# Kernel tuning notes

Hardware: AMD Instinct MI355X
Metric: run time of the kernel (lower is better)

## Reference

```python
import jax, jax.numpy as jnp
import numpy as np

# Model dims (see shape_source): seq_len fixed to 12 by reshape(1,12,-1); rnn_units fixed to 64 by proj in-dim.
B, T, N, HZ = 16, 12, 512, 12
DIN, DOUT, YCOV = 1, 1, 1
RNN, MEMN, MEMD, K = 64, 20, 64, 3
DDEC = RNN + MEMD  # 128


def _cheb(g, k):
    # Chebyshev polynomials T_0..T_{k-1} of support g: [I, g, 2g T_{i-1} - T_{i-2}, ...]
    n = g.shape[0]
    Ts = [jnp.eye(n, dtype=g.dtype), g]
    for _ in range(2, k):
        Ts.append(2.0 * g @ Ts[-1] - Ts[-2])
    return Ts


def _agcn(x, sup, W, b):
    # x: [B,N,C], sup: [2K,N,N] -> x_g: [B,N,2K*C] (k-major order matches torch.cat over support_set)
    b_, n, _ = x.shape
    xg = jnp.einsum('knm,bmc->bnkc', sup, x).reshape(b_, n, -1)
    return xg @ W + b


def _cell(x, state, sup, gW, gb, uW, ub, hdim):
    ins = jnp.concatenate([x, state], axis=-1)
    zr = jax.nn.sigmoid(_agcn(ins, sup, gW, gb))
    z, r = zr[..., :hdim], zr[..., hdim:]
    hc = jnp.tanh(_agcn(jnp.concatenate([x, z * state], axis=-1), sup, uW, ub))
    return r * state + (1.0 - r) * hc


def setup_inputs() -> dict:
    key = jax.random.key(0)
    ks = jax.random.split(key, 16)
    def nrm(k, shape, s=0.1):
        return jax.random.normal(k, shape, dtype=jnp.float32) * s
    return {
        'x': nrm(ks[0], (B, T, N, DIN), 1.0),
        'y_cov': nrm(ks[1], (B, HZ, N, YCOV), 1.0),
        'Memory': nrm(ks[2], (MEMN, MEMD)),
        'Wq': nrm(ks[3], (RNN, MEMD)),
        'We1': nrm(ks[4], (N, MEMN)),
        'We2': nrm(ks[5], (N, MEMN)),
        'tWe1': nrm(ks[6], (MEMD, RNN)),
        'tWe2': nrm(ks[7], (MEMD, RNN)),
        'fc_d_W': nrm(ks[8], (DDEC, RNN)),
        'fc_e_W': nrm(ks[9], (RNN, RNN)),
        'enc_gate_W': nrm(ks[10], (2 * K * (DIN + RNN), 2 * RNN)),
        'enc_gate_b': jnp.zeros((2 * RNN,), jnp.float32),
        'enc_up_W': nrm(ks[11], (2 * K * (DIN + RNN), RNN)),
        'enc_up_b': jnp.zeros((RNN,), jnp.float32),
        'dec_gate_W': nrm(ks[12], (2 * K * (DOUT + YCOV + DDEC), 2 * DDEC)),
        'dec_gate_b': jnp.zeros((2 * DDEC,), jnp.float32),
        'dec_up_W': nrm(ks[13], (2 * K * (DOUT + YCOV + DDEC), DDEC)),
        'dec_up_b': jnp.zeros((DDEC,), jnp.float32),
        'proj_W': nrm(ks[14], (DDEC + RNN, DOUT)),
        'proj_b': jnp.zeros((DOUT,), jnp.float32),
    }


def reference(x, y_cov, Memory, Wq, We1, We2, tWe1, tWe2, fc_d_W, fc_e_W,
              enc_gate_W, enc_gate_b, enc_up_W, enc_up_b,
              dec_gate_W, dec_gate_b, dec_up_W, dec_up_b, proj_W, proj_b):
    # adaptive supports from memory
    ne1 = We1 @ Memory
    ne2 = We2 @ Memory
    g1 = jax.nn.softmax(jax.nn.relu(ne1 @ ne2.T), axis=-1)
    g2 = jax.nn.softmax(jax.nn.relu(ne2 @ ne1.T), axis=-1)
    sup = jnp.stack(_cheb(g1, K) + _cheb(g2, K))  # [2K,N,N]

    # encoder: GRU-style graph recurrence over time via scan
    def enc_step(state, xt):
        h = _cell(xt, state, sup, enc_gate_W, enc_gate_b, enc_up_W, enc_up_b, RNN)
        return h, h
    s0 = jnp.zeros((B, N, RNN), x.dtype)
    _, hs = jax.lax.scan(enc_step, s0, jnp.swapaxes(x, 0, 1))
    h_en = jnp.swapaxes(hs, 0, 1)  # [B,T,N,RNN]
    h_t = h_en[:, -1]

    # memory retrieval
    query = h_t @ Wq                                    # [B,N,MEMD]
    att_score = jax.nn.softmax(query @ Memory.T, axis=-1)  # [B,N,MEMN]
    h_att = att_score @ Memory                          # [B,N,MEMD]
    _, ind = jax.lax.top_k(att_score, 20)
    pos = Memory[ind[:, :, 0]]
    neg = Memory[ind[:, :, 1:]]

    # test-time supports from last-batch retrieved memory (as in torch code: h_att[-1])
    ne3 = h_att[-1] @ tWe1
    ne4 = h_att[-1] @ tWe2
    tg1 = jax.nn.softmax(jax.nn.relu(ne3 @ ne4.T), axis=-1)
    tg2 = jax.nn.softmax(jax.nn.relu(ne4 @ ne3.T), axis=-1)
    tsup = jnp.stack(_cheb(tg1, K) + _cheb(tg2, K))

    ht = jnp.concatenate([h_t, h_att], axis=-1)  # [B,N,DDEC]
    # matches torch fc_e(h_en).reshape(1,12,-1): row-major flatten of [B,T,N,RNN] into [T, B*N*RNN]
    e_flat = (h_en @ fc_e_W).reshape(T, -1)

    go = jnp.zeros((B, N, DOUT), x.dtype)
    state = ht  # num_layers = 1
    outs = []
    for t in range(HZ):
        xt = jnp.concatenate([go, y_cov[:, t]], axis=-1)
        h_de = _cell(xt, state, tsup, dec_gate_W, dec_gate_b, dec_up_W, dec_up_b, DDEC)
        state = h_de
        d_flat = (h_de @ fc_d_W).reshape(-1)            # [B*N*RNN]
        att = jax.nn.softmax(e_flat @ d_flat)           # [T] global temporal weights
        context = jnp.einsum('btnr,t->bnr', h_en, att)  # [B,N,RNN]
        go = jnp.concatenate([h_de, context], axis=-1) @ proj_W + proj_b
        outs.append(go)
    output = jnp.stack(outs, axis=1)  # [B,HZ,N,DOUT]
    return output, h_att, query, pos, neg, att_score
```

## Files before the change

kernel.cpp:

```cpp
#include <hip/hip_runtime.h>
#include <hip/hip_bf16.h>
#include <math.h>

typedef __hip_bfloat16 bf16;
typedef __attribute__((ext_vector_type(8))) short short8;
typedef __attribute__((ext_vector_type(4))) float f32x4;
typedef unsigned short u16;

__device__ inline u16 f2bu(float f) {
  unsigned u = __builtin_bit_cast(unsigned, f);
  u += 0x7fffu + ((u >> 16) & 1u);
  return (u16)(u >> 16);
}

__global__ void detect_k(const u16* __restrict__ u, int* __restrict__ flag) {
  if (threadIdx.x == 0 && blockIdx.x == 0) {
    int wild = 0;
    for (int i = 0; i < 256; i++) {
      int e = (u[i] >> 7) & 0xFF;
      if (e < 0x66 || e > 0x8A) wild++;
    }
    *flag = (wild > 64) ? 1 : 0;
  }
}

__global__ void in2f_k(const void* __restrict__ in, float* __restrict__ out, int n,
                       const int* __restrict__ flag) {
  int i = blockIdx.x * 256 + threadIdx.x;
  if (i >= n) return;
  if (*flag) out[i] = ((const float*)in)[i];
  else       out[i] = __bfloat162float(((const bf16*)in)[i]);
}

__global__ void zero_k(float* __restrict__ p, int n) {
  int i = blockIdx.x * 256 + threadIdx.x;
  if (i < n) p[i] = 0.f;
}

__global__ void zeroi_k(int* __restrict__ p, int n) {
  int i = blockIdx.x * 256 + threadIdx.x;
  if (i < n) p[i] = 0;
}

__global__ void transpose_k(const float* __restrict__ in, float* __restrict__ out,
                            int rows, int cols) {
  int i = blockIdx.x * 256 + threadIdx.x;
  if (i >= rows * cols) return;
  int c = i % cols, r = i / cols;
  out[(size_t)c * rows + r] = in[i];
}

__global__ void f2b_k(const float* __restrict__ in, u16* __restrict__ out, int n) {
  int i = blockIdx.x * 256 + threadIdx.x;
  if (i < n) out[i] = f2bu(in[i]);
}

__global__ void padw_k(const float* __restrict__ W, float* __restrict__ Wp,
                       int K, int N, int Kpad) {
  int i = blockIdx.x * 256 + threadIdx.x;
  if (i >= Kpad * N) return;
  int n = i % N, k = i / N;
  Wp[i] = (k < K) ? W[(size_t)k * N + n] : 0.f;
}

__global__ void w2bt_k(const float* __restrict__ W, u16* __restrict__ WT,
                       int KT, int Nw, int KTpad) {
  int i = blockIdx.x * 256 + threadIdx.x;
  if (i >= Nw * KTpad) return;
  int kp = i % KTpad, n = i / KTpad;
  WT[i] = (kp < KT) ? f2bu(W[(size_t)kp * Nw + n]) : (u16)0;
}

enum { EPI_NONE = 0, EPI_RELU = 1, EPI_SIG = 2, EPI_CHEB = 3, EPI_SCAT = 4, EPI_UPD = 5 };

struct GemmArgs {
  const float* A; const float* Bm; float* C;
  int M, N, K;
};
__global__ __launch_bounds__(256) void gemm_s(GemmArgs g) {
  __shared__ float As[16][65];
  __shared__ float Bs[16][65];
  const int tid = threadIdx.x;
  const int tx = tid & 15, ty = tid >> 4;
  const int bm = blockIdx.y * 64, bn = blockIdx.x * 64;
  float acc[4][4] = {{0.f}};
  for (int k0 = 0; k0 < g.K; k0 += 16) {
#pragma unroll
    for (int i = 0; i < 4; i++) {
      int idx = i * 256 + tid; int c = idx & 15, r = idx >> 4;
      int mm = bm + r, kk = k0 + c;
      As[c][r] = (mm < g.M && kk < g.K) ? g.A[(size_t)mm * g.K + kk] : 0.f;
    }
#pragma unroll
    for (int i = 0; i < 4; i++) {
      int idx = i * 256 + tid; int c = idx & 63, r = idx >> 6;
      int kk = k0 + r, nn = bn + c;
      Bs[r][c] = (kk < g.K && nn < g.N) ? g.Bm[(size_t)kk * g.N + nn] : 0.f;
    }
    __syncthreads();
#pragma unroll
    for (int kk = 0; kk < 16; kk++) {
      float a[4], b[4];
#pragma unroll
      for (int i = 0; i < 4; i++) a[i] = As[kk][ty * 4 + i];
#pragma unroll
      for (int j = 0; j < 4; j++) b[j] = Bs[kk][tx * 4 + j];
#pragma unroll
      for (int i = 0; i < 4; i++)
#pragma unroll
        for (int j = 0; j < 4; j++) acc[i][j] = fmaf(a[i], b[j], acc[i][j]);
    }
    __syncthreads();
  }
#pragma unroll
  for (int i = 0; i < 4; i++) {
    int m = bm + ty * 4 + i;
    if (m >= g.M) continue;
#pragma unroll
    for (int j = 0; j < 4; j++) {
      int n = bn + tx * 4 + j;
      if (n >= g.N) continue;
      g.C[(size_t)m * g.N + n] = acc[i][j];
    }
  }
}

struct FGemmArgs {
  const float* A; const float* Bm; const float* bias; float* C;
  int M, N, K, ldb;
  const float* aux0;
  float* aux1;
  float* aux2;
  float* aux3;
  float* aux4;
  int i0, i1, i2;
};

template<int EPI>
__global__ __launch_bounds__(256) void fgemm_k(FGemmArgs g) {
  __shared__ __align__(16) float As[2][32][68];
  __shared__ __align__(16) float Bs[2][32][68];
  const int tid = threadIdx.x;
  const int tx = tid & 15, ty = tid >> 4;
  const int bm = blockIdx.y * 64, bn = blockIdx.x * 64;
  const int ar = tid >> 2, ac = (tid & 3) * 4;
  const int br = tid >> 4, bc = (tid & 15) * 4;
  float acc[4][4] = {{0.f}};

  float4 av0 = *(const float4*)(g.A + (size_t)(bm + ar) * g.K + ac);
  float4 av1 = *(const float4*)(g.A + (size_t)(bm + ar) * g.K + 16 + ac);
  float4 bv0 = *(const float4*)(g.Bm + (size_t)br * g.ldb + bn + bc);
  float4 bv1 = *(const float4*)(g.Bm + (size_t)(16 + br) * g.ldb + bn + bc);
  As[0][ac + 0][ar] = av0.x; As[0][ac + 1][ar] = av0.y;
  As[0][ac + 2][ar] = av0.z; As[0][ac + 3][ar] = av0.w;
  As[0][16 + ac + 0][ar] = av1.x; As[0][16 + ac + 1][ar] = av1.y;
  As[0][16 + ac + 2][ar] = av1.z; As[0][16 + ac + 3][ar] = av1.w;
  *(float4*)&Bs[0][br][bc] = bv0;
  *(float4*)&Bs[0][16 + br][bc] = bv1;
  __syncthreads();

  int cur = 0;
  for (int k0 = 0; k0 < g.K; k0 += 32) {
    const bool has_next = (k0 + 32 < g.K);
    if (has_next) {
      av0 = *(const float4*)(g.A + (size_t)(bm + ar) * g.K + k0 + 32 + ac);
      av1 = *(const float4*)(g.A + (size_t)(bm + ar) * g.K + k0 + 48 + ac);
      bv0 = *(const float4*)(g.Bm + (size_t)(k0 + 32 + br) * g.ldb + bn + bc);
      bv1 = *(const float4*)(g.Bm + (size_t)(k0 + 48 + br) * g.ldb + bn + bc);
    }
#pragma unroll
    for (int kk = 0; kk < 32; kk++) {
      float4 a4 = *(const float4*)&As[cur][kk][ty * 4];
      float4 b4 = *(const float4*)&Bs[cur][kk][tx * 4];
      float a[4] = {a4.x, a4.y, a4.z, a4.w};
      float b[4] = {b4.x, b4.y, b4.z, b4.w};
#pragma unroll
      for (int i = 0; i < 4; i++)
#pragma unroll
        for (int j = 0; j < 4; j++) acc[i][j] = fmaf(a[i], b[j], acc[i][j]);
    }
    if (has_next) {
      int nxt = cur ^ 1;
      As[nxt][ac + 0][ar] = av0.x; As[nxt][ac + 1][ar] = av0.y;
      As[nxt][ac + 2][ar] = av0.z; As[nxt][ac + 3][ar] = av0.w;
      As[nxt][16 + ac + 0][ar] = av1.x; As[nxt][16 + ac + 1][ar] = av1.y;
      As[nxt][16 + ac + 2][ar] = av1.z; As[nxt][16 + ac + 3][ar] = av1.w;
      *(float4*)&Bs[nxt][br][bc] = bv0;
      *(float4*)&Bs[nxt][16 + br][bc] = bv1;
      __syncthreads();
      cur = nxt;
    }
  }
#pragma unroll
  for (int i = 0; i < 4; i++) {
    int m = bm + ty * 4 + i;
#pragma unroll
    for (int j = 0; j < 4; j++) {
      int n = bn + tx * 4 + j;
      if (n >= g.N) continue;
      float v = acc[i][j];
      if (EPI == EPI_NONE) {
        g.C[(size_t)m * g.N + n] = v;
      } else if (EPI == EPI_RELU) {
        g.C[(size_t)m * g.N + n] = fmaxf(v, 0.f);
      } else if (EPI == EPI_CHEB) {
        g.C[(size_t)m * g.N + n] = 2.f * v - (m == n ? 1.f : 0.f);
      } else if (EPI == EPI_SCAT) {
        int bb = n / g.i0, cc = n % g.i0;
        int km = m >> 9;
        int kmap = km + 1 + (km >= 2 ? 1 : 0);
        int node = m & 511;
        g.aux1[((size_t)bb * 512 + node) * g.i1 + (size_t)kmap * g.i0 + cc] = v;
      }
    }
  }
}

template<int EPI>
__global__ __launch_bounds__(256) void fgemm32_k(FGemmArgs g) {
  __shared__ __align__(16) float As[2][16][40];
  __shared__ __align__(16) float Bs[2][16][68];
  const int tid = threadIdx.x;
  const int tx = tid & 15, ty = tid >> 4;
  const int bm = blockIdx.y * 32, bn = blockIdx.x * 64;
  const int ar = tid >> 2, ac = (tid & 3) * 4;
  const int br = tid >> 4, bc = (tid & 15) * 4;
  float acc[2][4] = {{0.f}};

  float4 av, bv;
  if (ar < 32) av = *(const float4*)(g.A + (size_t)(bm + ar) * g.K + ac);
  bv = *(const float4*)(g.Bm + (size_t)br * g.ldb + bn + bc);
  if (ar < 32) {
    As[0][ac + 0][ar] = av.x; As[0][ac + 1][ar] = av.y;
    As[0][ac + 2][ar] = av.z; As[0][ac + 3][ar] = av.w;
  }
  *(float4*)&Bs[0][br][bc] = bv;
  __syncthreads();

  int cur = 0;
  for (int k0 = 0; k0 < g.K; k0 += 16) {
    const bool has_next = (k0 + 16 < g.K);
    if (has_next) {
      if (ar < 32) av = *(const float4*)(g.A + (size_t)(bm + ar) * g.K + k0 + 16 + ac);
      bv = *(const float4*)(g.Bm + (size_t)(k0 + 16 + br) * g.ldb + bn + bc);
    }
#pragma unroll
    for (int kk = 0; kk < 16; kk++) {
      float a0 = As[cur][kk][ty * 2 + 0];
      float a1 = As[cur][kk][ty * 2 + 1];
      float4 b4 = *(const float4*)&Bs[cur][kk][tx * 4];
      float b[4] = {b4.x, b4.y, b4.z, b4.w};
#pragma unroll
      for (int j = 0; j < 4; j++) {
        acc[0][j] = fmaf(a0, b[j], acc[0][j]);
        acc[1][j] = fmaf(a1, b[j], acc[1][j]);
      }
    }
    if (has_next) {
      int nxt = cur ^ 1;
      if (ar < 32) {
        As[nxt][ac + 0][ar] = av.x; As[nxt][ac + 1][ar] = av.y;
        As[nxt][ac + 2][ar] = av.z; As[nxt][ac + 3][ar] = av.w;
      }
      *(float4*)&Bs[nxt][br][bc] = bv;
      __syncthreads();
      cur = nxt;
    }
  }
#pragma unroll
  for (int i = 0; i < 2; i++) {
    int m = bm + ty * 2 + i;
    int node = m & 511, bb = m >> 9;
#pragma unroll
    for (int j = 0; j < 4; j++) {
      int n = bn + tx * 4 + j;
      if (n >= g.N) continue;
      float v = acc[i][j];
      if (EPI == EPI_NONE) {
        g.C[(size_t)m * g.N + n] = v;
      } else if (EPI == EPI_RELU) {
        g.C[(size_t)m * g.N + n] = fmaxf(v, 0.f);
      } else if (EPI == EPI_CHEB) {
        g.C[(size_t)m * g.N + n] = 2.f * v - (m == n ? 1.f : 0.f);
      } else if (EPI == EPI_SCAT) {
        int b2 = n / g.i0, cc = n % g.i0;
        int km = m >> 9;
        int kmap = km + 1 + (km >= 2 ? 1 : 0);
        g.aux1[((size_t)b2 * 512 + node) * g.i1 + (size_t)kmap * g.i0 + cc] = v;
      } else if (EPI == EPI_SIG) {
        v += g.bias[n];
        float sg = 1.f / (1.f + expf(-v));
        g.C[(size_t)m * g.N + n] = sg;
        if (n < 64) {
          float zh = sg * g.aux0[(size_t)m * 64 + n];
          g.aux3[(size_t)node * 1088 + bb * 65 + 1 + n] = zh;
          g.aux4[(size_t)m * 416 + 1 + n] = zh;
          g.aux4[(size_t)m * 416 + 196 + n] = zh;
        }
      } else if (EPI == EPI_UPD) {
        v = tanhf(v + g.bias[n]);
        float r = g.aux0[(size_t)m * g.i0 + g.i1 + n];
        float h = r * g.aux1[(size_t)m * g.i1 + n] + (1.f - r) * v;
        g.aux1[(size_t)m * g.i1 + n] = h;
        if (g.aux2)
          g.aux2[(((size_t)bb * 12 + g.i2) * 512 + node) * 64 + n] = h;
        g.aux3[(size_t)node * 1088 + bb * 65 + 1 + n] = h;
        g.aux4[(size_t)m * 416 + 1 + n] = h;
        g.aux4[(size_t)m * 416 + 196 + n] = h;
      }
    }
  }
}

struct MmArgs {
  const u16* A; const u16* BT; int M, N, K;
  const float* bias; float* C;
  u16* xg;
  const float* zr; float* state; float* hen;
  u16* xtw; u16* xgw;
  int i0, i1, i2;
};

template<int EPI>
__global__ __launch_bounds__(256) void mm_k(MmArgs g) {
  __shared__ __align__(16) u16 Als[2][64][40];
  __shared__ __align__(16) u16 Bls[2][64][40];
  const int tid = threadIdx.x;
  const int w = tid >> 6, lane = tid & 63;
  const int l15 = lane & 15, lk = lane >> 4;
  const int m0 = blockIdx.y * 64, n0 = blockIdx.x * 64;
  const int srow = tid >> 2, schunk = tid & 3;
  f32x4 acc[4];
#pragma unroll
  for (int j = 0; j < 4; j++) acc[j] = (f32x4){0.f, 0.f, 0.f, 0.f};

  short8 a8 = *(const short8*)(g.A + (size_t)(m0 + srow) * g.K + schunk * 8);
  short8 b8 = (short8){0,0,0,0,0,0,0,0};
  if (n0 + srow < g.N)
    b8 = *(const short8*)(g.BT + (size_t)(n0 + srow) * g.K + schunk * 8);
  *(short8*)&Als[0][srow][schunk * 8] = a8;
  *(short8*)&Bls[0][srow][schunk * 8] = b8;
  __syncthreads();

  int cur = 0;
  for (int k0 = 0; k0 < g.K; k0 += 32) {
    const bool has_next = (k0 + 32 < g.K);
    if (has_next) {
      a8 = *(const short8*)(g.A + (size_t)(m0 + srow) * g.K + k0 + 32 + schunk * 8);
      b8 = (short8){0,0,0,0,0,0,0,0};
      if (n0 + srow < g.N)
        b8 = *(const short8*)(g.BT + (size_t)(n0 + srow) * g.K + k0 + 32 + schunk * 8);
    }
    short8 af = *(const short8*)&Als[cur][w * 16 + l15][lk * 8];
#pragma unroll
    for (int j = 0; j < 4; j++) {
      short8 bf = *(const short8*)&Bls[cur][j * 16 + l15][lk * 8];
      acc[j] = __builtin_amdgcn_mfma_f32_16x16x32_bf16(af, bf, acc[j], 0, 0, 0);
    }
    if (has_next) {
      int nxt = cur ^ 1;
      *(short8*)&Als[nxt][srow][schunk * 8] = a8;
      *(short8*)&Bls[nxt][srow][schunk * 8] = b8;
      __syncthreads();
      cur = nxt;
    }
  }

#pragma unroll
  for (int j = 0; j < 4; j++) {
    int col = n0 + j * 16 + l15;
    if (col >= g.N) continue;
#pragma unroll
    for (int r = 0; r < 4; r++) {
      int row = m0 + w * 16 + lk * 4 + r;
      int node = row & 511, bb = row >> 9;
      float v = acc[j][r];
      if (EPI == EPI_SCAT) {
        int b2 = col / g.i0, cc = col % g.i0;
        int km = row >> 9;
        int kmap = km + 1 + (km >= 2 ? 1 : 0);
        g.xg[((size_t)b2 * 512 + node) * g.i1 + (size_t)kmap * g.i0 + cc] = f2bu(v);
      } else if (EPI == EPI_SIG) {
        v += g.bias[col];
        float sg = 1.f / (1.f + expf(-v));
        g.C[(size_t)row * g.N + col] = sg;
        if (col < 128) {
          float zh = sg * g.state[(size_t)row * 128 + col];
          u16 bv = f2bu(zh);
          g.xtw[((size_t)(bb * 130 + 2 + col)) * 512 + node] = bv;
          g.xgw[(size_t)row * 800 + 2 + col] = bv;
          g.xgw[(size_t)row * 800 + 392 + col] = bv;
        }
      } else if (EPI == EPI_UPD) {
        v = tanhf(v + g.bias[col]);
        float rr = g.zr[(size_t)row * g.i0 + g.i1 + col];
        float h = rr * g.state[(size_t)row * g.i1 + col] + (1.f - rr) * v;
        g.state[(size_t)row * g.i1 + col] = h;
        u16 bv = f2bu(h);
        g.xtw[((size_t)(bb * 130 + 2 + col)) * 512 + node] = bv;
        g.xgw[(size_t)row * 800 + 2 + col] = bv;
        g.xgw[(size_t)row * 800 + 392 + col] = bv;
      }
    }
  }
}


__global__ void putxe_k(const float* __restrict__ x1, float* __restrict__ X,
                        float* __restrict__ XG) {
  int bn = blockIdx.x * 256 + threadIdx.x;
  if (bn >= 8192) return;
  int n = bn & 511, b = bn >> 9;
  float v = x1[(size_t)b * 6144 + n];
  X[(size_t)n * 1088 + b * 65] = v;
  XG[(size_t)bn * 416 + 0] = v;
  XG[(size_t)bn * 416 + 195] = v;
}

__global__ void putxd_k(const float* __restrict__ yc, u16* __restrict__ XT,
                        u16* __restrict__ XGb) {
  int bn = blockIdx.x * 256 + threadIdx.x;
  if (bn >= 8192) return;
  int n = bn & 511, b = bn >> 9;
  u16 bv = f2bu(yc[(size_t)b * 6144 + n]);
  XT[((size_t)(b * 130 + 1)) * 512 + n] = bv;
  XGb[(size_t)bn * 800 + 1] = bv;
  XGb[(size_t)bn * 800 + 391] = bv;
}

__global__ __launch_bounds__(256) void softmax512_k(const float* __restrict__ Min,
                                                    float* __restrict__ out, int colMajor) {
  int row = blockIdx.x;
  __shared__ float buf[512];
  __shared__ float red[256];
  int tid = threadIdx.x;
  for (int i = tid; i < 512; i += 256)
    buf[i] = colMajor ? Min[(size_t)i * 512 + row] : Min[(size_t)row * 512 + i];
  __syncthreads();
  float mx = -1e30f;
  for (int i = tid; i < 512; i += 256) mx = fmaxf(mx, buf[i]);
  red[tid] = mx; __syncthreads();
  for (int w = 128; w > 0; w >>= 1) { if (tid < w) red[tid] = fmaxf(red[tid], red[tid + w]); __syncthreads(); }
  mx = red[0]; __syncthreads();
  float s = 0.f;
  for (int i = tid; i < 512; i += 256) { float e = expf(buf[i] - mx); buf[i] = e; s += e; }
  red[tid] = s; __syncthreads();
  for (int w = 128; w > 0; w >>= 1) { if (tid < w) red[tid] += red[tid + w]; __syncthreads(); }
  float inv = 1.f / red[0];
  for (int i = tid; i < 512; i += 256) out[(size_t)row * 512 + i] = buf[i] * inv;
}

__global__ __launch_bounds__(256) void attmem_k(const float* __restrict__ query,
    const float* __restrict__ Mem, float* __restrict__ att_out,
    float* __restrict__ hatt, int* __restrict__ ind) {
  __shared__ float sm[20 * 64];
  for (int i = threadIdx.x; i < 20 * 64; i += 256) sm[i] = Mem[i];
  __syncthreads();
  int bn = blockIdx.x * 256 + threadIdx.x;
  if (bn >= 16 * 512) return;
  float q[64];
#pragma unroll
  for (int d = 0; d < 64; d++) q[d] = query[(size_t)bn * 64 + d];
  float lg[20];
  float mx = -1e30f;
#pragma unroll
  for (int m = 0; m < 20; m++) {
    float s = 0.f;
#pragma unroll
    for (int d = 0; d < 64; d++) s = fmaf(q[d], sm[m * 64 + d], s);
    lg[m] = s; mx = fmaxf(mx, s);
  }
  float se = 0.f;
#pragma unroll
  for (int m = 0; m < 20; m++) { lg[m] = expf(lg[m] - mx); se += lg[m]; }
  float inv = 1.f / se;
#pragma unroll
  for (int m = 0; m < 20; m++) {
    lg[m] *= inv;
    att_out[(size_t)bn * 20 + m] = lg[m];
  }
#pragma unroll
  for (int d = 0; d < 64; d++) {
    float s = 0.f;
#pragma unroll
    for (int m = 0; m < 20; m++) s = fmaf(lg[m], sm[m * 64 + d], s);
    hatt[(size_t)bn * 64 + d] = s;
  }
  unsigned used = 0;
  for (int s = 0; s < 20; s++) {
    float bv = -1e30f; int bi = 0;
#pragma unroll
    for (int m = 0; m < 20; m++) {
      bool better = (!((used >> m) & 1u)) && (lg[m] > bv);
      if (better) { bv = lg[m]; bi = m; }
    }
    used |= (1u << bi);
    ind[(size_t)bn * 20 + s] = bi;
  }
}

__global__ void gather_pn_k(const int* __restrict__ ind, const float* __restrict__ Memf,
                            float* __restrict__ pos, float* __restrict__ neg) {
  size_t i = (size_t)blockIdx.x * 256 + threadIdx.x;
  if (i >= (size_t)16 * 512 * 20 * 64) return;
  int d = (int)(i & 63); size_t r = i >> 6;
  int s = (int)(r % 20); size_t bn = r / 20;
  int m = ind[bn * 20 + s];
  float v = Memf[m * 64 + d];
  if (s == 0) pos[bn * 64 + d] = v;
  else neg[(bn * 19 + (size_t)(s - 1)) * 64 + d] = v;
}

__global__ void sinit_k(const float* __restrict__ H, const float* __restrict__ hatt,
                        float* __restrict__ S, u16* __restrict__ XT,
                        u16* __restrict__ XGb) {
  int i = blockIdx.x * 256 + threadIdx.x;
  if (i >= 8192 * 128) return;
  int c = i & 127; int bn = i >> 7;
  int n = bn & 511, b = bn >> 9;
  float v = (c < 64) ? H[(size_t)bn * 64 + c] : hatt[(size_t)bn * 64 + (c - 64)];
  S[i] = v;
  u16 bv = f2bu(v);
  XT[((size_t)(b * 130 + 2 + c)) * 512 + n] = bv;
  XGb[(size_t)bn * 800 + 2 + c] = bv;
  XGb[(size_t)bn * 800 + 392 + c] = bv;
  if (c == 0) {
    XT[((size_t)(b * 130)) * 512 + n] = 0;
  }
}

__global__ __launch_bounds__(256) void att_dot_k(const float* __restrict__ E,
    const float* __restrict__ D, float* __restrict__ partial) {
  int t = blockIdx.y, ch = blockIdx.x;
  const float* e = E + (size_t)t * 524288 + (size_t)ch * 16384;
  const float* d = D + (size_t)ch * 16384;
  float s = 0.f;
  for (int i = threadIdx.x; i < 16384; i += 256) s = fmaf(e[i], d[i], s);
  __shared__ float red[256];
  red[threadIdx.x] = s; __syncthreads();
  for (int w = 128; w > 0; w >>= 1) {
    if (threadIdx.x < w) red[threadIdx.x] += red[threadIdx.x + w];
    __syncthreads();
  }
  if (threadIdx.x == 0) partial[t * 32 + ch] = red[0];
}

__global__ __launch_bounds__(64) void ctxgo_k(const float* __restrict__ hen,
    const float* __restrict__ partial, const float* __restrict__ S,
    const float* __restrict__ pW, const float* __restrict__ pb,
    u16* __restrict__ XT, u16* __restrict__ XGb,
    float* __restrict__ outp, int tstep) {
  int bn = blockIdx.x; int r = threadIdx.x;
  __shared__ float a[12];
  __shared__ float l[12];
  if (r < 12) {
    float s = 0.f;
    for (int i = 0; i < 32; i++) s += partial[r * 32 + i];
    l[r] = s;
  }
  __syncthreads();
  if (r == 0) {
    float mx = l[0];
    for (int i = 1; i < 12; i++) mx = fmaxf(mx, l[i]);
    float se = 0.f; float e[12];
    for (int i = 0; i < 12; i++) { e[i] = expf(l[i] - mx); se += e[i]; }
    float inv = 1.f / se;
    for (int i = 0; i < 12; i++) a[i] = e[i] * inv;
  }
  __syncthreads();
  int b = bn >> 9, n = bn & 511;
  float ctx = 0.f;
#pragma unroll
  for (int t = 0; t < 12; t++)
    ctx = fmaf(hen[((size_t)(b * 12 + t) * 512 + n) * 64 + r], a[t], ctx);
  float part = ctx * pW[128 + r] + S[(size_t)bn * 128 + r] * pW[r]
             + S[(size_t)bn * 128 + 64 + r] * pW[64 + r];
#pragma unroll
  for (int off = 32; off > 0; off >>= 1) part += __shfl_down(part, off);
  if (r == 0) {
    float gv = part + pb[0];
    outp[(size_t)(b * 12 + tstep) * 512 + n] = gv;
    u16 bv = f2bu(gv);
    XT[((size_t)(b * 130)) * 512 + n] = bv;
    XGb[(size_t)bn * 800 + 0] = bv;
    XGb[(size_t)bn * 800 + 390] = bv;
  }
}


static void fgemm(hipStream_t st, int epi, const float* A, const float* Bm,
                  const float* bias, float* C, int M, int N, int K, int ldb,
                  const float* aux0, float* aux1, float* aux2, float* aux3, float* aux4,
                  int i0, int i1, int i2) {
  FGemmArgs a{A, Bm, bias, C, M, N, K, ldb, aux0, aux1, aux2, aux3, aux4, i0, i1, i2};
  dim3 grid((N + 63) / 64, M / 64);
  switch (epi) {
    case 0: fgemm_k<0><<<grid, 256, 0, st>>>(a); break;
    case 1: fgemm_k<1><<<grid, 256, 0, st>>>(a); break;
    case 3: fgemm_k<3><<<grid, 256, 0, st>>>(a); break;
    case 4: fgemm_k<4><<<grid, 256, 0, st>>>(a); break;
  }
}

static void fgemm32(hipStream_t st, int epi, const float* A, const float* Bm,
                    const float* bias, float* C, int M, int N, int K, int ldb,
                    const float* aux0, float* aux1, float* aux2, float* aux3, float* aux4,
                    int i0, int i1, int i2) {
  FGemmArgs a{A, Bm, bias, C, M, N, K, ldb, aux0, aux1, aux2, aux3, aux4, i0, i1, i2};
  dim3 grid((N + 63) / 64, M / 32);
  switch (epi) {
    case 0: fgemm32_k<0><<<grid, 256, 0, st>>>(a); break;
    case 1: fgemm32_k<1><<<grid, 256, 0, st>>>(a); break;
    case 2: fgemm32_k<2><<<grid, 256, 0, st>>>(a); break;
    case 3: fgemm32_k<3><<<grid, 256, 0, st>>>(a); break;
    case 4: fgemm32_k<4><<<grid, 256, 0, st>>>(a); break;
    case 5: fgemm32_k<5><<<grid, 256, 0, st>>>(a); break;
  }
}

static void mm(hipStream_t st, int epi, const u16* A, const u16* BT,
               int M, int N, int K, const float* bias, float* C, u16* xg,
               const float* zr, float* state, float* hen, u16* xtw, u16* xgw,
               int i0, int i1, int i2) {
  MmArgs a{A, BT, M, N, K, bias, C, xg, zr, state, hen, xtw, xgw, i0, i1, i2};
  dim3 grid((N + 63) / 64, M / 64);
  switch (epi) {
    case EPI_SIG:  mm_k<EPI_SIG><<<grid, 256, 0, st>>>(a); break;
    case EPI_SCAT: mm_k<EPI_SCAT><<<grid, 256, 0, st>>>(a); break;
    case EPI_UPD:  mm_k<EPI_UPD><<<grid, 256, 0, st>>>(a); break;
  }
}

extern "C" void kernel_launch(void* const* d_in, const int* in_sizes, int n_in,
                              void* d_out, int out_size, void* d_ws, size_t ws_size,
                              hipStream_t stream) {
  (void)out_size; (void)ws_size; (void)n_in; (void)in_sizes;
  float* ws = (float*)d_ws;
  float* out = (float*)d_out;

  size_t off = 0;
  auto alloc = [&](size_t n) { size_t o = off; off += (n + 63) & ~(size_t)63; return ws + o; };

  const int isz[20] = {98304, 98304, 1280, 4096, 10240, 10240, 4096, 4096, 8192, 4096,
                       49920, 128, 24960, 64, 199680, 256, 99840, 128, 192, 1};
  float* fin[20];
  for (int i = 0; i < 20; i++) fin[i] = alloc((size_t)isz[i]);

  float* Gbig  = alloc((size_t)2048 * 512);
  float* tGbig = Gbig;
  float* Mbuf  = alloc((size_t)512 * 512);
  float* ne1b  = alloc((size_t)512 * 64);
  float* ne2b  = alloc((size_t)512 * 64);
  float* neT   = alloc((size_t)64 * 512);
  float* X     = alloc((size_t)512 * 1088);
  float* XG    = alloc((size_t)8192 * 416);
  float* Wgp   = alloc((size_t)416 * 128);
  float* Wup   = alloc((size_t)416 * 64);
  float* zr    = alloc((size_t)8192 * 256);
  float* H     = alloc((size_t)8192 * 64);
  float* S     = alloc((size_t)8192 * 128);
  float* hen   = alloc((size_t)16 * 12 * 512 * 64);
  float* E     = alloc((size_t)16 * 12 * 512 * 64);
  float* Dflat = alloc((size_t)8192 * 64);
  float* partial = alloc((size_t)512);
  int* ind     = (int*)alloc((size_t)8192 * 20);
  int* dflag   = (int*)alloc((size_t)64);
  u16* Gb16 = (u16*)alloc((size_t)2048 * 512 / 2);
  u16* XT   = (u16*)alloc((size_t)2080 * 512 / 2);
  u16* XGb  = (u16*)alloc((size_t)8192 * 800 / 2);
  u16* WTdg = (u16*)alloc((size_t)256 * 800 / 2);
  u16* WTdu = (u16*)alloc((size_t)128 * 800 / 2);

  float* o_out   = out;
  float* o_hatt  = out + 98304;
  float* o_query = o_hatt + 524288;
  float* o_pos   = o_query + 524288;
  float* o_neg   = o_pos + 524288;
  float* o_att   = o_neg + 9961472;

  detect_k<<<1, 64, 0, stream>>>((const u16*)d_in[0], dflag);
  for (int i = 0; i < 20; i++)
    in2f_k<<<(isz[i] + 255) / 256, 256, 0, stream>>>(d_in[i], fin[i], isz[i], dflag);

  padw_k<<<(416 * 128 + 255) / 256, 256, 0, stream>>>(fin[10], Wgp, 390, 128, 416);
  padw_k<<<(416 * 64 + 255) / 256, 256, 0, stream>>>(fin[12], Wup, 390, 64, 416);
  w2bt_k<<<(256 * 800 + 255) / 256, 256, 0, stream>>>(fin[14], WTdg, 780, 256, 800);
  w2bt_k<<<(128 * 800 + 255) / 256, 256, 0, stream>>>(fin[16], WTdu, 780, 128, 800);

  zero_k<<<(512 * 1088 + 255) / 256, 256, 0, stream>>>(X, 512 * 1088);
  zero_k<<<(8192 * 416 + 255) / 256, 256, 0, stream>>>(XG, 8192 * 416);

  {
    GemmArgs a1{fin[4], fin[2], ne1b, 512, 64, 20};
    gemm_s<<<dim3(1, 8), 256, 0, stream>>>(a1);
    GemmArgs a2{fin[5], fin[2], ne2b, 512, 64, 20};
    gemm_s<<<dim3(1, 8), 256, 0, stream>>>(a2);
  }
  transpose_k<<<(512 * 64 + 255) / 256, 256, 0, stream>>>(ne2b, neT, 512, 64);
  fgemm32(stream, EPI_RELU, ne1b, neT, nullptr, Mbuf, 512, 512, 64, 512,
          nullptr, nullptr, nullptr, nullptr, nullptr, 0, 0, 0);
  softmax512_k<<<512, 256, 0, stream>>>(Mbuf, Gbig, 0);
  softmax512_k<<<512, 256, 0, stream>>>(Mbuf, Gbig + (size_t)1024 * 512, 1);
  fgemm32(stream, EPI_CHEB, Gbig, Gbig, nullptr, Gbig + (size_t)512 * 512,
          512, 512, 512, 512, nullptr, nullptr, nullptr, nullptr, nullptr, 0, 0, 0);
  fgemm32(stream, EPI_CHEB, Gbig + (size_t)1024 * 512, Gbig + (size_t)1024 * 512, nullptr,
          Gbig + (size_t)1536 * 512, 512, 512, 512, 512,
          nullptr, nullptr, nullptr, nullptr, nullptr, 0, 0, 0);

  zero_k<<<(8192 * 64 + 255) / 256, 256, 0, stream>>>(H, 8192 * 64);

  for (int t = 0; t < 12; t++) {
    putxe_k<<<32, 256, 0, stream>>>(fin[0] + t * 512, X, XG);
    fgemm32(stream, EPI_SCAT, Gbig, X, nullptr, nullptr, 2048, 1040, 512, 1088,
            nullptr, XG, nullptr, nullptr, nullptr, 65, 416, 0);
    fgemm32(stream, EPI_SIG, XG, Wgp, fin[11], zr, 8192, 128, 416, 128,
            H, nullptr, nullptr, X, XG, 0, 0, 0);
    fgemm32(stream, EPI_SCAT, Gbig, X, nullptr, nullptr, 2048, 1040, 512, 1088,
            nullptr, XG, nullptr, nullptr, nullptr, 65, 416, 0);
    fgemm32(stream, EPI_UPD, XG, Wup, fin[13], nullptr, 8192, 64, 416, 64,
            zr, H, hen, X, XG, 128, 64, t);
  }

  fgemm(stream, EPI_NONE, H, fin[3], nullptr, o_query, 8192, 64, 64, 64,
        nullptr, nullptr, nullptr, nullptr, nullptr, 0, 0, 0);
  attmem_k<<<32, 256, 0, stream>>>(o_query, fin[2], o_att, o_hatt, ind);
  gather_pn_k<<<(16 * 512 * 20 * 64 + 255) / 256, 256, 0, stream>>>(
      ind, fin[2], o_pos, o_neg);

  fgemm(stream, EPI_NONE, hen, fin[9], nullptr, E, 98304, 64, 64, 64,
        nullptr, nullptr, nullptr, nullptr, nullptr, 0, 0, 0);

  fgemm(stream, EPI_NONE, o_hatt + (size_t)15 * 512 * 64, fin[6], nullptr, ne1b,
        512, 64, 64, 64, nullptr, nullptr, nullptr, nullptr, nullptr, 0, 0, 0);
  fgemm(stream, EPI_NONE, o_hatt + (size_t)15 * 512 * 64, fin[7], nullptr, ne2b,
        512, 64, 64, 64, nullptr, nullptr, nullptr, nullptr, nullptr, 0, 0, 0);
  transpose_k<<<(512 * 64 + 255) / 256, 256, 0, stream>>>(ne2b, neT, 512, 64);
  fgemm32(stream, EPI_RELU, ne1b, neT, nullptr, Mbuf, 512, 512, 64, 512,
          nullptr, nullptr, nullptr, nullptr, nullptr, 0, 0, 0);
  softmax512_k<<<512, 256, 0, stream>>>(Mbuf, tGbig, 0);
  softmax512_k<<<512, 256, 0, stream>>>(Mbuf, tGbig + (size_t)1024 * 512, 1);
  fgemm32(stream, EPI_CHEB, tGbig, tGbig, nullptr, tGbig + (size_t)512 * 512,
          512, 512, 512, 512, nullptr, nullptr, nullptr, nullptr, nullptr, 0, 0, 0);
  fgemm32(stream, EPI_CHEB, tGbig + (size_t)1024 * 512, tGbig + (size_t)1024 * 512, nullptr,
          tGbig + (size_t)1536 * 512, 512, 512, 512, 512,
          nullptr, nullptr, nullptr, nullptr, nullptr, 0, 0, 0);
  f2b_k<<<(2048 * 512 + 255) / 256, 256, 0, stream>>>(tGbig, Gb16, 2048 * 512);

  zeroi_k<<<(8192 * 800 / 2 + 255) / 256, 256, 0, stream>>>((int*)XGb, 8192 * 800 / 2);
  sinit_k<<<(8192 * 128 + 255) / 256, 256, 0, stream>>>(H, o_hatt, S, XT, XGb);

  for (int t = 0; t < 12; t++) {
    putxd_k<<<32, 256, 0, stream>>>(fin[1] + t * 512, XT, XGb);
    mm(stream, EPI_SCAT, Gb16, XT, 2048, 2080, 512, nullptr, nullptr, XGb,
       nullptr, nullptr, nullptr, nullptr, nullptr, 130, 800, 0);
    mm(stream, EPI_SIG, XGb, WTdg, 8192, 256, 800, fin[15], zr, nullptr,
       nullptr, S, nullptr, XT, XGb, 0, 0, 0);
    mm(stream, EPI_SCAT, Gb16, XT, 2048, 2080, 512, nullptr, nullptr, XGb,
       nullptr, nullptr, nullptr, nullptr, nullptr, 130, 800, 0);
    mm(stream, EPI_UPD, XGb, WTdu, 8192, 128, 800, fin[17], nullptr, nullptr,
       zr, S, nullptr, XT, XGb, 256, 128, 0);
    fgemm32(stream, EPI_NONE, S, fin[8], nullptr, Dflat, 8192, 64, 128, 64,
            nullptr, nullptr, nullptr, nullptr, nullptr, 0, 0, 0);
    att_dot_k<<<dim3(32, 12), 256, 0, stream>>>(E, Dflat, partial);
    ctxgo_k<<<8192, 64, 0, stream>>>(hen, partial, S, fin[18], fin[19],
                                     XT, XGb, o_out, t);
  }
}
```

Baseline: 3.575 ms.

## Drop input dtype detection and conversion; shrink fgemm k-tile; use 64-row scatter GEMM

New measurement: 3.358 ms. 1.06x faster.

```diff
diff --git a/kernel.cpp b/kernel.cpp
--- a/kernel.cpp
+++ b/kernel.cpp
@@ -11,25 +11,6 @@
   unsigned u = __builtin_bit_cast(unsigned, f);
   u += 0x7fffu + ((u >> 16) & 1u);
   return (u16)(u >> 16);
-}
-
-__global__ void detect_k(const u16* __restrict__ u, int* __restrict__ flag) {
-  if (threadIdx.x == 0 && blockIdx.x == 0) {
-    int wild = 0;
-    for (int i = 0; i < 256; i++) {
-      int e = (u[i] >> 7) & 0xFF;
-      if (e < 0x66 || e > 0x8A) wild++;
-    }
-    *flag = (wild > 64) ? 1 : 0;
-  }
-}
-
-__global__ void in2f_k(const void* __restrict__ in, float* __restrict__ out, int n,
-                       const int* __restrict__ flag) {
-  int i = blockIdx.x * 256 + threadIdx.x;
-  if (i >= n) return;
-  if (*flag) out[i] = ((const float*)in)[i];
-  else       out[i] = __bfloat162float(((const bf16*)in)[i]);
 }
 
 __global__ void zero_k(float* __restrict__ p, int n) {
@@ -138,8 +119,8 @@
 
 template<int EPI>
 __global__ __launch_bounds__(256) void fgemm_k(FGemmArgs g) {
-  __shared__ __align__(16) float As[2][32][68];
-  __shared__ __align__(16) float Bs[2][32][68];
+  __shared__ __align__(16) float As[2][16][68];
+  __shared__ __align__(16) float Bs[2][16][68];
   const int tid = threadIdx.x;
   const int tx = tid & 15, ty = tid >> 4;
   const int bm = blockIdx.y * 64, bn = blockIdx.x * 64;
@@ -147,29 +128,22 @@
   const int br = tid >> 4, bc = (tid & 15) * 4;
   float acc[4][4] = {{0.f}};
 
-  float4 av0 = *(const float4*)(g.A + (size_t)(bm + ar) * g.K + ac);
-  float4 av1 = *(const float4*)(g.A + (size_t)(bm + ar) * g.K + 16 + ac);
-  float4 bv0 = *(const float4*)(g.Bm + (size_t)br * g.ldb + bn + bc);
-  float4 bv1 = *(const float4*)(g.Bm + (size_t)(16 + br) * g.ldb + bn + bc);
-  As[0][ac + 0][ar] = av0.x; As[0][ac + 1][ar] = av0.y;
-  As[0][ac + 2][ar] = av0.z; As[0][ac + 3][ar] = av0.w;
-  As[0][16 + ac + 0][ar] = av1.x; As[0][16 + ac + 1][ar] = av1.y;
-  As[0][16 + ac + 2][ar] = av1.z; As[0][16 + ac + 3][ar] = av1.w;
-  *(float4*)&Bs[0][br][bc] = bv0;
-  *(float4*)&Bs[0][16 + br][bc] = bv1;
+  float4 av = *(const float4*)(g.A + (size_t)(bm + ar) * g.K + ac);
+  float4 bv = *(const float4*)(g.Bm + (size_t)br * g.ldb + bn + bc);
+  As[0][ac + 0][ar] = av.x; As[0][ac + 1][ar] = av.y;
+  As[0][ac + 2][ar] = av.z; As[0][ac + 3][ar] = av.w;
+  *(float4*)&Bs[0][br][bc] = bv;
   __syncthreads();
 
   int cur = 0;
-  for (int k0 = 0; k0 < g.K; k0 += 32) {
-    const bool has_next = (k0 + 32 < g.K);
+  for (int k0 = 0; k0 < g.K; k0 += 16) {
+    const bool has_next = (k0 + 16 < g.K);
     if (has_next) {
-      av0 = *(const float4*)(g.A + (size_t)(bm + ar) * g.K + k0 + 32 + ac);
-      av1 = *(const float4*)(g.A + (size_t)(bm + ar) * g.K + k0 + 48 + ac);
-      bv0 = *(const float4*)(g.Bm + (size_t)(k0 + 32 + br) * g.ldb + bn + bc);
-      bv1 = *(const float4*)(g.Bm + (size_t)(k0 + 48 + br) * g.ldb + bn + bc);
-    }
-#pragma unroll
-    for (int kk = 0; kk < 32; kk++) {
+      av = *(const float4*)(g.A + (size_t)(bm + ar) * g.K + k0 + 16 + ac);
+      bv = *(const float4*)(g.Bm + (size_t)(k0 + 16 + br) * g.ldb + bn + bc);
+    }
+#pragma unroll
+    for (int kk = 0; kk < 16; kk++) {
       float4 a4 = *(const float4*)&As[cur][kk][ty * 4];
       float4 b4 = *(const float4*)&Bs[cur][kk][tx * 4];
       float a[4] = {a4.x, a4.y, a4.z, a4.w};
@@ -181,12 +155,9 @@
     }
     if (has_next) {
       int nxt = cur ^ 1;
-      As[nxt][ac + 0][ar] = av0.x; As[nxt][ac + 1][ar] = av0.y;
-      As[nxt][ac + 2][ar] = av0.z; As[nxt][ac + 3][ar] = av0.w;
-      As[nxt][16 + ac + 0][ar] = av1.x; As[nxt][16 + ac + 1][ar] = av1.y;
-      As[nxt][16 + ac + 2][ar] = av1.z; As[nxt][16 + ac + 3][ar] = av1.w;
-      *(float4*)&Bs[nxt][br][bc] = bv0;
-      *(float4*)&Bs[nxt][16 + br][bc] = bv1;
+      As[nxt][ac + 0][ar] = av.x; As[nxt][ac + 1][ar] = av.y;
+      As[nxt][ac + 2][ar] = av.z; As[nxt][ac + 3][ar] = av.w;
+      *(float4*)&Bs[nxt][br][bc] = bv;
       __syncthreads();
       cur = nxt;
     }
@@ -282,11 +253,6 @@
         g.C[(size_t)m * g.N + n] = fmaxf(v, 0.f);
       } else if (EPI == EPI_CHEB) {
         g.C[(size_t)m * g.N + n] = 2.f * v - (m == n ? 1.f : 0.f);
-      } else if (EPI == EPI_SCAT) {
-        int b2 = n / g.i0, cc = n % g.i0;
-        int km = m >> 9;
-        int kmap = km + 1 + (km >= 2 ? 1 : 0);
-        g.aux1[((size_t)b2 * 512 + node) * g.i1 + (size_t)kmap * g.i0 + cc] = v;
       } else if (EPI == EPI_SIG) {
         v += g.bias[n];
         float sg = 1.f / (1.f + expf(-v));
@@ -613,7 +579,6 @@
     case 1: fgemm32_k<1><<<grid, 256, 0, st>>>(a); break;
     case 2: fgemm32_k<2><<<grid, 256, 0, st>>>(a); break;
     case 3: fgemm32_k<3><<<grid, 256, 0, st>>>(a); break;
-    case 4: fgemm32_k<4><<<grid, 256, 0, st>>>(a); break;
     case 5: fgemm32_k<5><<<grid, 256, 0, st>>>(a); break;
   }
 }
@@ -638,13 +603,29 @@
   float* ws = (float*)d_ws;
   float* out = (float*)d_out;
 
+  const float* in_x    = (const float*)d_in[0];
+  const float* in_ycov = (const float*)d_in[1];
+  const float* in_mem  = (const float*)d_in[2];
+  const float* in_wq   = (const float*)d_in[3];
+  const float* in_we1  = (const float*)d_in[4];
+  const float* in_we2  = (const float*)d_in[5];
+  const float* in_twe1 = (const float*)d_in[6];
+  const float* in_twe2 = (const float*)d_in[7];
+  const float* in_fcd  = (const float*)d_in[8];
+  const float* in_fce  = (const float*)d_in[9];
+  const float* in_egW  = (const float*)d_in[10];
+  const float* in_egb  = (const float*)d_in[11];
+  const float* in_euW  = (const float*)d_in[12];
+  const float* in_eub  = (const float*)d_in[13];
+  const float* in_dgW  = (const float*)d_in[14];
+  const float* in_dgb  = (const float*)d_in[15];
+  const float* in_duW  = (const float*)d_in[16];
+  const float* in_dub  = (const float*)d_in[17];
+  const float* in_pW   = (const float*)d_in[18];
+  const float* in_pb   = (const float*)d_in[19];
+
   size_t off = 0;
   auto alloc = [&](size_t n) { size_t o = off; off += (n + 63) & ~(size_t)63; return ws + o; };
-
-  const int isz[20] = {98304, 98304, 1280, 4096, 10240, 10240, 4096, 4096, 8192, 4096,
-                       49920, 128, 24960, 64, 199680, 256, 99840, 128, 192, 1};
-  float* fin[20];
-  for (int i = 0; i < 20; i++) fin[i] = alloc((size_t)isz[i]);
 
   float* Gbig  = alloc((size_t)2048 * 512);
   float* tGbig = Gbig;
@@ -664,7 +645,6 @@
   float* Dflat = alloc((size_t)8192 * 64);
   float* partial = alloc((size_t)512);
   int* ind     = (int*)alloc((size_t)8192 * 20);
-  int* dflag   = (int*)alloc((size_t)64);
   u16* Gb16 = (u16*)alloc((size_t)2048 * 512 / 2);
   u16* XT   = (u16*)alloc((size_t)2080 * 512 / 2);
   u16* XGb  = (u16*)alloc((size_t)8192 * 800 / 2);
@@ -678,22 +658,18 @@
   float* o_neg   = o_pos + 524288;
   float* o_att   = o_neg + 9961472;
 
-  detect_k<<<1, 64, 0, stream>>>((const u16*)d_in[0], dflag);
-  for (int i = 0; i < 20; i++)
-    in2f_k<<<(isz[i] + 255) / 256, 256, 0, stream>>>(d_in[i], fin[i], isz[i], dflag);
-
-  padw_k<<<(416 * 128 + 255) / 256, 256, 0, stream>>>(fin[10], Wgp, 390, 128, 416);
-  padw_k<<<(416 * 64 + 255) / 256, 256, 0, stream>>>(fin[12], Wup, 390, 64, 416);
-  w2bt_k<<<(256 * 800 + 255) / 256, 256, 0, stream>>>(fin[14], WTdg, 780, 256, 800);
-  w2bt_k<<<(128 * 800 + 255) / 256, 256, 0, stream>>>(fin[16], WTdu, 780, 128, 800);
+  padw_k<<<(416 * 128 + 255) / 256, 256, 0, stream>>>(in_egW, Wgp, 390, 128, 416);
+  padw_k<<<(416 * 64 + 255) / 256, 256, 0, stream>>>(in_euW, Wup, 390, 64, 416);
+  w2bt_k<<<(256 * 800 + 255) / 256, 256, 0, stream>>>(in_dgW, WTdg, 780, 256, 800);
+  w2bt_k<<<(128 * 800 + 255) / 256, 256, 0, stream>>>(in_duW, WTdu, 780, 128, 800);
 
   zero_k<<<(512 * 1088 + 255) / 256, 256, 0, stream>>>(X, 512 * 1088);
   zero_k<<<(8192 * 416 + 255) / 256, 256, 0, stream>>>(XG, 8192 * 416);
 
   {
-    GemmArgs a1{fin[4], fin[2], ne1b, 512, 64, 20};
+    GemmArgs a1{in_we1, in_mem, ne1b, 512, 64, 20};
     gemm_s<<<dim3(1, 8), 256, 0, stream>>>(a1);
-    GemmArgs a2{fin[5], fin[2], ne2b, 512, 64, 20};
+    GemmArgs a2{in_we2, in_mem, ne2b, 512, 64, 20};
     gemm_s<<<dim3(1, 8), 256, 0, stream>>>(a2);
   }
   transpose_k<<<(512 * 64 + 255) / 256, 256, 0, stream>>>(ne2b, neT, 512, 64);
@@ -710,29 +686,29 @@
   zero_k<<<(8192 * 64 + 255) / 256, 256, 0, stream>>>(H, 8192 * 64);
 
   for (int t = 0; t < 12; t++) {
-    putxe_k<<<32, 256, 0, stream>>>(fin[0] + t * 512, X, XG);
-    fgemm32(stream, EPI_SCAT, Gbig, X, nullptr, nullptr, 2048, 1040, 512, 1088,
-            nullptr, XG, nullptr, nullptr, nullptr, 65, 416, 0);
-    fgemm32(stream, EPI_SIG, XG, Wgp, fin[11], zr, 8192, 128, 416, 128,
+    putxe_k<<<32, 256, 0, stream>>>(in_x + t * 512, X, XG);
+    fgemm(stream, EPI_SCAT, Gbig, X, nullptr, nullptr, 2048, 1040, 512, 1088,
+          nullptr, XG, nullptr, nullptr, nullptr, 65, 416, 0);
+    fgemm32(stream, EPI_SIG, XG, Wgp, in_egb, zr, 8192, 128, 416, 128,
             H, nullptr, nullptr, X, XG, 0, 0, 0);
-    fgemm32(stream, EPI_SCAT, Gbig, X, nullptr, nullptr, 2048, 1040, 512, 1088,
-            nullptr, XG, nullptr, nullptr, nullptr, 65, 416, 0);
-    fgemm32(stream, EPI_UPD, XG, Wup, fin[13], nullptr, 8192, 64, 416, 64,
+    fgemm(stream, EPI_SCAT, Gbig, X, nullptr, nullptr, 2048, 1040, 512, 1088,
+          nullptr, XG, nullptr, nullptr, nullptr, 65, 416, 0);
+    fgemm32(stream, EPI_UPD, XG, Wup, in_eub, nullptr, 8192, 64, 416, 64,
             zr, H, hen, X, XG, 128, 64, t);
   }
 
-  fgemm(stream, EPI_NONE, H, fin[3], nullptr, o_query, 8192, 64, 64, 64,
+  fgemm(stream, EPI_NONE, H, in_wq, nullptr, o_query, 8192, 64, 64, 64,
         nullptr, nullptr, nullptr, nullptr, nullptr, 0, 0, 0);
-  attmem_k<<<32, 256, 0, stream>>>(o_query, fin[2], o_att, o_hatt, ind);
+  attmem_k<<<32, 256, 0, stream>>>(o_query, in_mem, o_att, o_hatt, ind);
   gather_pn_k<<<(16 * 512 * 20 * 64 + 255) / 256, 256, 0, stream>>>(
-      ind, fin[2], o_pos, o_neg);
-
-  fgemm(stream, EPI_NONE, hen, fin[9], nullptr, E, 98304, 64, 64, 64,
+      ind, in_mem, o_pos, o_neg);
+
+  fgemm(stream, EPI_NONE, hen, in_fce, nullptr, E, 98304, 64, 64, 64,
         nullptr, nullptr, nullptr, nullptr, nullptr, 0, 0, 0);
 
-  fgemm(stream, EPI_NONE, o_hatt + (size_t)15 * 512 * 64, fin[6], nullptr, ne1b,
+  fgemm(stream, EPI_NONE, o_hatt + (size_t)15 * 512 * 64, in_twe1, nullptr, ne1b,
         512, 64, 64, 64, nullptr, nullptr, nullptr, nullptr, nullptr, 0, 0, 0);
-  fgemm(stream, EPI_NONE, o_hatt + (size_t)15 * 512 * 64, fin[7], nullptr, ne2b,
+  fgemm(stream, EPI_NONE, o_hatt + (size_t)15 * 512 * 64, in_twe2, nullptr, ne2b,
         512, 64, 64, 64, nullptr, nullptr, nullptr, nullptr, nullptr, 0, 0, 0);
   transpose_k<<<(512 * 64 + 255) / 256, 256, 0, stream>>>(ne2b, neT, 512, 64);
   fgemm32(stream, EPI_RELU, ne1b, neT, nullptr, Mbuf, 512, 512, 64, 512,
@@ -750,19 +726,19 @@
   sinit_k<<<(8192 * 128 + 255) / 256, 256, 0, stream>>>(H, o_hatt, S, XT, XGb);
 
   for (int t = 0; t < 12; t++) {
-    putxd_k<<<32, 256, 0, stream>>>(fin[1] + t * 512, XT, XGb);
+    putxd_k<<<32, 256, 0, stream>>>(in_ycov + t * 512, XT, XGb);
     mm(stream, EPI_SCAT, Gb16, XT, 2048, 2080, 512, nullptr, nullptr, XGb,
        nullptr, nullptr, nullptr, nullptr, nullptr, 130, 800, 0);
-    mm(stream, EPI_SIG, XGb, WTdg, 8192, 256, 800, fin[15], zr, nullptr,
+    mm(stream, EPI_SIG, XGb, WTdg, 8192, 256, 800, in_dgb, zr, nullptr,
        nullptr, S, nullptr, XT, XGb, 0, 0, 0);
     mm(stream, EPI_SCAT, Gb16, XT, 2048, 2080, 512, nullptr, nullptr, XGb,
        nullptr, nullptr, nullptr, nullptr, nullptr, 130, 800, 0);
-    mm(stream, EPI_UPD, XGb, WTdu, 8192, 128, 800, fin[17], nullptr, nullptr,
+    mm(stream, EPI_UPD, XGb, WTdu, 8192, 128, 800, in_dub, nullptr, nullptr,
        zr, S, nullptr, XT, XGb, 256, 128, 0);
-    fgemm32(stream, EPI_NONE, S, fin[8], nullptr, Dflat, 8192, 64, 128, 64,
+    fgemm32(stream, EPI_NONE, S, in_fcd, nullptr, Dflat, 8192, 64, 128, 64,
             nullptr, nullptr, nullptr, nullptr, nullptr, 0, 0, 0);
     att_dot_k<<<dim3(32, 12), 256, 0, stream>>>(E, Dflat, partial);
-    ctxgo_k<<<8192, 64, 0, stream>>>(hen, partial, S, fin[18], fin[19],
+    ctxgo_k<<<8192, 64, 0, stream>>>(hen, partial, S, in_pW, in_pb,
                                      XT, XGb, o_out, t);
   }
 }
```
